# Performance work log

Measured on AMD Instinct MI355X. Metric: run time of the kernel, lower is better.

The kernel has to match this reference:

```python
import jax, jax.numpy as jnp
import numpy as np

UNITS = 128  # rnn_units hardcoded in the module


def setup_inputs() -> dict:
    key = jax.random.key(0)
    k1, k2, k3 = jax.random.split(key, 3)
    B, T, F = 256, 1024, 128  # feature dim must equal UNITS (shared cell across both layers)
    inputs = jax.random.normal(k1, (B, T, F), dtype=jnp.float32)
    # Keras LSTMCell params, gate order i|f|g|o; SHARED by both stacked layers
    # because StackedRNNCells([cell]*2) reuses the same cell object.
    W = jax.random.normal(k2, (F, 4 * UNITS), dtype=jnp.float32) * 0.05   # kernel
    U = jax.random.normal(k3, (UNITS, 4 * UNITS), dtype=jnp.float32) * 0.05  # recurrent_kernel
    b = jnp.zeros((4 * UNITS,), dtype=jnp.float32)  # bias
    return {"inputs": inputs, "W": W, "U": U, "b": b}


def _lstm_cell(x, h, c, W, U, b):
    # z: [B, 4*UNITS]; Keras gate order i, f, g(candidate), o
    z = x @ W + h @ U + b
    i, f, g, o = jnp.split(z, 4, axis=-1)
    i = jax.nn.sigmoid(i)
    f = jax.nn.sigmoid(f)
    g = jnp.tanh(g)
    o = jax.nn.sigmoid(o)
    c_new = f * c + i * g
    h_new = o * jnp.tanh(c_new)
    return h_new, c_new


def reference(inputs, W, U, b):
    B, T, F = inputs.shape
    z0 = jnp.zeros((B, UNITS), dtype=inputs.dtype)

    def step(carry, x_t):
        h1, c1, h2, c2 = carry
        h1, c1 = _lstm_cell(x_t, h1, c1, W, U, b)   # layer 1
        h2, c2 = _lstm_cell(h1, h2, c2, W, U, b)    # layer 2 (shared weights)
        return (h1, c1, h2, c2), None

    (h1, c1, h2, c2), _ = jax.lax.scan(step, (z0, z0, z0, z0), jnp.swapaxes(inputs, 0, 1))
    outputs = h2                                    # last-step output (return_sequences=False)
    init_state = jnp.zeros(inputs.shape, dtype=inputs.dtype)  # tf.zeros(inputs.shape)
    final_state = c1  # source unpacks `outputs, _, h2, _, _` -> 2nd flat state = layer-1 cell state
    return (outputs, init_state, final_state)
```

## Files before the change

### kernel.cpp

```cpp
#include <hip/hip_runtime.h>


typedef _Float16 f16;
typedef _Float16 f16x2 __attribute__((ext_vector_type(2)));
typedef _Float16 f16x8 __attribute__((ext_vector_type(8)));
typedef float    f32x4 __attribute__((ext_vector_type(4)));

#define T_STEPS 1024
#define UNITS   128
#define NB      32
#define BPW     8
#define NBLK    256
#define OUT_ZERO 32768
#define OUT_C1   33587200
#define BUFB     6144

__device__ __forceinline__ float frcp_(float x) {
#if __has_builtin(__builtin_amdgcn_rcpf)
    return __builtin_amdgcn_rcpf(x);
#else
    return 1.0f / x;
#endif
}
__device__ __forceinline__ float sigmoidf_(float x) {
    return frcp_(1.0f + __expf(-x));
}
__device__ __forceinline__ float tanhf_(float x) {
    float e = __expf(2.0f * x);
    return 1.0f - 2.0f * frcp_(e + 1.0f);
}
__device__ __forceinline__ unsigned pkh(float a, float b) {
    f16x2 t; t[0] = (f16)a; t[1] = (f16)b;
    return __builtin_bit_cast(unsigned, t);
}

__global__ __launch_bounds__(512, 2) void lstm2_kernel(
    const float* __restrict__ X,
    const float* __restrict__ W,
    const float* __restrict__ U,
    const float* __restrict__ Bv,
    float* __restrict__ out)
{
    const int blk = blockIdx.x;
    const int tid = threadIdx.x;

    if (blk >= NB) {
        const size_t nthr = (size_t)(NBLK - NB) * 512;
        float4* dst = (float4*)(out + OUT_ZERO);
        const float4 z4 = make_float4(0.f, 0.f, 0.f, 0.f);
        for (size_t i = (size_t)(blk - NB) * 512 + tid; i < 8388608u; i += nthr)
            dst[i] = z4;
        return;
    }

    const int wv = tid >> 6;
    const int l  = tid & 63;
    const int lr = l & 15;
    const int lc = l >> 4;
    const int u  = wv * 16 + lr;
    const int b0 = blk * BPW;
    const bool cell2 = (l >= 32);

    __shared__ __align__(16) char Abuf[2][BUFB];
    char* Ab = (char*)Abuf;

    f16x8 Wf[4][4], Uf[4][4];
    #pragma unroll
    for (int g = 0; g < 4; ++g) {
        #pragma unroll
        for (int kt = 0; kt < 4; ++kt) {
            f16x8 wt, ut;
            #pragma unroll
            for (int j = 0; j < 8; ++j) {
                const int krow = kt * 32 + lc * 8 + j;
                wt[j] = (f16)W[(size_t)krow * 512 + g * 128 + u];
                ut[j] = (f16)U[(size_t)krow * 512 + g * 128 + u];
            }
            Wf[g][kt] = wt;  Uf[g][kt] = ut;
        }
    }
    float bias[4];
    #pragma unroll
    for (int g = 0; g < 4; ++g) bias[g] = Bv[g * 128 + u];

    const int swz = (lr & 7) << 4;
    int raddr[2][4];
    #pragma unroll
    for (int a0 = 0; a0 < 2; ++a0)
        #pragma unroll
        for (int kt = 0; kt < 4; ++kt)
            raddr[a0][kt] = (((a0 * 8 + lr) * 256) + kt * 64 + lc * 16) ^ swz;
    int waddr[4];
    #pragma unroll
    for (int e = 0; e < 4; ++e)
        waddr[e] = ((8 + 4 * lc + e) * 256 + u * 2) ^ ((((4 * lc + e) & 7)) << 4);

    for (int i = tid; i < 3072; i += 512) ((float*)Ab)[i] = 0.0f;
    {
        const int flat = tid * 2, xr = flat >> 7, xc = flat & 127;
        const float2 xv = *(const float2*)(X + (size_t)(b0 + xr) * (T_STEPS * UNITS) + xc);
        const int byte = ((xr * 256 + xc * 2) ^ ((xr & 7) << 4));
        *(unsigned*)(Ab + byte) = pkh(xv.x, xv.y);
    }
    __syncthreads();

    float cst[4] = {0.f, 0.f, 0.f, 0.f};

    for (int k = 0; k <= T_STEPS; ++k) {
        const int rdo = (k & 1) * BUFB, wro = BUFB - rdo;

        float xa = 0.f, xb = 0.f; int xr = 0, xc = 0;
        if (k + 1 < T_STEPS) {
            const int flat = tid * 2; xr = flat >> 7; xc = flat & 127;
            const float2 xv = *(const float2*)(X + (size_t)(b0 + xr) * (T_STEPS * UNITS)
                                                 + (size_t)(k + 1) * UNITS + xc);
            xa = xv.x; xb = xv.y;
        }

        f16x8 A1[4], A2[4];
        #pragma unroll
        for (int kt = 0; kt < 4; ++kt) {
            A1[kt] = *(const f16x8*)(Ab + rdo + raddr[0][kt]);
            A2[kt] = *(const f16x8*)(Ab + rdo + raddr[1][kt]);
        }

        f32x4 acc[4];
        #pragma unroll
        for (int g = 0; g < 4; ++g) acc[g] = f32x4{0.f, 0.f, 0.f, 0.f};
        #pragma unroll
        for (int kt = 0; kt < 4; ++kt)
            #pragma unroll
            for (int g = 0; g < 4; ++g)
                acc[g] = __builtin_amdgcn_mfma_f32_16x16x32_f16(A1[kt], Wf[g][kt], acc[g], 0, 0, 0);
        #pragma unroll
        for (int kt = 0; kt < 4; ++kt)
            #pragma unroll
            for (int g = 0; g < 4; ++g)
                acc[g] = __builtin_amdgcn_mfma_f32_16x16x32_f16(A2[kt], Uf[g][kt], acc[g], 0, 0, 0);

        const bool active = cell2 ? (k > 0) : (k < T_STEPS);
        float hq[4];
        #pragma unroll
        for (int e = 0; e < 4; ++e) {
            const float zi = acc[0][e] + bias[0];
            const float zf = acc[1][e] + bias[1];
            const float zg = acc[2][e] + bias[2];
            const float zo = acc[3][e] + bias[3];
            const float ig = sigmoidf_(zi), fg = sigmoidf_(zf);
            const float gg = tanhf_(zg),    og = sigmoidf_(zo);
            const float cn = fg * cst[e] + ig * gg;
            if (active) cst[e] = cn;
            hq[e] = og * tanhf_(cn);
        }

        if (active && k < T_STEPS) {
            #pragma unroll
            for (int e = 0; e < 4; ++e)
                *(f16*)(Ab + wro + waddr[e]) = (f16)hq[e];
        }
        if (k + 1 < T_STEPS) {
            const int byte = ((xr * 256 + xc * 2) ^ ((xr & 7) << 4));
            *(unsigned*)(Ab + wro + byte) = pkh(xa, xb);
        }

        if (k == T_STEPS - 1 && !cell2) {
            #pragma unroll
            for (int e = 0; e < 4; ++e)
                out[OUT_C1 + (size_t)(b0 + 4 * lc + e) * UNITS + u] = cst[e];
        }
        if (k == T_STEPS && cell2) {
            #pragma unroll
            for (int e = 0; e < 4; ++e)
                out[(size_t)(b0 + 4 * lc + e - 8) * UNITS + u] = hq[e];
        }
        __syncthreads();
    }
}

extern "C" void kernel_launch(void* const* d_in, const int* in_sizes, int n_in,
                              void* d_out, int out_size, void* d_ws, size_t ws_size,
                              hipStream_t stream) {
    const float* X  = (const float*)d_in[0];
    const float* W  = (const float*)d_in[1];
    const float* U  = (const float*)d_in[2];
    const float* Bv = (const float*)d_in[3];
    float* out = (float*)d_out;
    hipLaunchKernelGGL(lstm2_kernel, dim3(NBLK), dim3(512), 0, stream,
                       X, W, U, Bv, out);
}
```

Measured before the change: 1.186 ms.

## Use 64 LSTM blocks with 4 batches each and a fused K=256 MFMA

```diff
diff --git a/kernel.cpp b/kernel.cpp
--- a/kernel.cpp
+++ b/kernel.cpp
@@ -8,12 +8,13 @@
 
 #define T_STEPS 1024
 #define UNITS   128
-#define NB      32
-#define BPW     8
+#define NLSTM   64
+#define BPW     4
 #define NBLK    256
 #define OUT_ZERO 32768
 #define OUT_C1   33587200
-#define BUFB     6144
+#define ROWB    512
+#define ABUF_B  (16*ROWB)
 
 __device__ __forceinline__ float frcp_(float x) {
 #if __has_builtin(__builtin_amdgcn_rcpf)
@@ -33,6 +34,13 @@
     f16x2 t; t[0] = (f16)a; t[1] = (f16)b;
     return __builtin_bit_cast(unsigned, t);
 }
+__device__ __forceinline__ unsigned short hbits(float a) {
+    f16 t = (f16)a;
+    return __builtin_bit_cast(unsigned short, t);
+}
+__device__ __forceinline__ int swb(int row, int byteoff) {
+    return row * ROWB + ((((byteoff >> 4) ^ (row & 7)) << 4) | (byteoff & 15));
+}
 
 __global__ __launch_bounds__(512, 2) void lstm2_kernel(
     const float* __restrict__ X,
@@ -44,135 +52,124 @@
     const int blk = blockIdx.x;
     const int tid = threadIdx.x;
 
-    if (blk >= NB) {
-        const size_t nthr = (size_t)(NBLK - NB) * 512;
+    if (blk >= NLSTM) {
+        const size_t nthr = (size_t)(NBLK - NLSTM) * 512;
         float4* dst = (float4*)(out + OUT_ZERO);
         const float4 z4 = make_float4(0.f, 0.f, 0.f, 0.f);
-        for (size_t i = (size_t)(blk - NB) * 512 + tid; i < 8388608u; i += nthr)
+        for (size_t i = (size_t)(blk - NLSTM) * 512 + tid; i < 8388608u; i += nthr)
             dst[i] = z4;
         return;
     }
 
-    const int wv = tid >> 6;
+    const int w  = tid >> 6;
     const int l  = tid & 63;
     const int lr = l & 15;
     const int lc = l >> 4;
-    const int u  = wv * 16 + lr;
+    const int u  = w * 16 + lr;
     const int b0 = blk * BPW;
-    const bool cell2 = (l >= 32);
 
-    __shared__ __align__(16) char Abuf[2][BUFB];
-    char* Ab = (char*)Abuf;
+    __shared__ __align__(16) char   Ab[2][ABUF_B];
+    __shared__ __align__(16) float4 zlds[8][129];
 
-    f16x8 Wf[4][4], Uf[4][4];
+    f16x8 Bf[4][8];
     #pragma unroll
     for (int g = 0; g < 4; ++g) {
         #pragma unroll
-        for (int kt = 0; kt < 4; ++kt) {
-            f16x8 wt, ut;
+        for (int kt = 0; kt < 8; ++kt) {
+            f16x8 t;
             #pragma unroll
             for (int j = 0; j < 8; ++j) {
-                const int krow = kt * 32 + lc * 8 + j;
-                wt[j] = (f16)W[(size_t)krow * 512 + g * 128 + u];
-                ut[j] = (f16)U[(size_t)krow * 512 + g * 128 + u];
+                const int kg = kt * 32 + lc * 8 + j;
+                const float v = (kg < 128) ? W[(size_t)kg * 512 + g * 128 + u]
+                                           : U[(size_t)(kg - 128) * 512 + g * 128 + u];
+                t[j] = (f16)v;
             }
-            Wf[g][kt] = wt;  Uf[g][kt] = ut;
+            Bf[g][kt] = t;
         }
     }
     float bias[4];
     #pragma unroll
     for (int g = 0; g < 4; ++g) bias[g] = Bv[g * 128 + u];
 
-    const int swz = (lr & 7) << 4;
-    int raddr[2][4];
-    #pragma unroll
-    for (int a0 = 0; a0 < 2; ++a0)
-        #pragma unroll
-        for (int kt = 0; kt < 4; ++kt)
-            raddr[a0][kt] = (((a0 * 8 + lr) * 256) + kt * 64 + lc * 16) ^ swz;
-    int waddr[4];
-    #pragma unroll
-    for (int e = 0; e < 4; ++e)
-        waddr[e] = ((8 + 4 * lc + e) * 256 + u * 2) ^ ((((4 * lc + e) & 7)) << 4);
-
-    for (int i = tid; i < 3072; i += 512) ((float*)Ab)[i] = 0.0f;
-    {
+    for (int i = tid; i < 2 * ABUF_B / 16; i += 512) ((float4*)Ab)[i] = make_float4(0.f,0.f,0.f,0.f);
+    __syncthreads();
+    if (tid < 256) {
         const int flat = tid * 2, xr = flat >> 7, xc = flat & 127;
         const float2 xv = *(const float2*)(X + (size_t)(b0 + xr) * (T_STEPS * UNITS) + xc);
-        const int byte = ((xr * 256 + xc * 2) ^ ((xr & 7) << 4));
-        *(unsigned*)(Ab + byte) = pkh(xv.x, xv.y);
+        *(unsigned*)(&Ab[0][0] + swb(xr, xc * 2)) = pkh(xv.x, xv.y);
     }
     __syncthreads();
 
-    float cst[4] = {0.f, 0.f, 0.f, 0.f};
+    int ard[8];
+    #pragma unroll
+    for (int kt = 0; kt < 8; ++kt) ard[kt] = swb(lr, kt * 64 + lc * 16);
+
+    float c1 = 0.f, c2 = 0.f;
 
     for (int k = 0; k <= T_STEPS; ++k) {
-        const int rdo = (k & 1) * BUFB, wro = BUFB - rdo;
+        const int rdo = (k & 1) * ABUF_B, wro = ABUF_B - rdo;
+        char* Abr = &Ab[0][0] + rdo;
+        char* Abw = &Ab[0][0] + wro;
 
         float xa = 0.f, xb = 0.f; int xr = 0, xc = 0;
-        if (k + 1 < T_STEPS) {
+        if (tid < 256 && k + 1 < T_STEPS) {
             const int flat = tid * 2; xr = flat >> 7; xc = flat & 127;
             const float2 xv = *(const float2*)(X + (size_t)(b0 + xr) * (T_STEPS * UNITS)
                                                  + (size_t)(k + 1) * UNITS + xc);
             xa = xv.x; xb = xv.y;
         }
 
-        f16x8 A1[4], A2[4];
+        f16x8 Af[8];
         #pragma unroll
-        for (int kt = 0; kt < 4; ++kt) {
-            A1[kt] = *(const f16x8*)(Ab + rdo + raddr[0][kt]);
-            A2[kt] = *(const f16x8*)(Ab + rdo + raddr[1][kt]);
-        }
+        for (int kt = 0; kt < 8; ++kt) Af[kt] = *(const f16x8*)(Abr + ard[kt]);
 
         f32x4 acc[4];
         #pragma unroll
         for (int g = 0; g < 4; ++g) acc[g] = f32x4{0.f, 0.f, 0.f, 0.f};
         #pragma unroll
-        for (int kt = 0; kt < 4; ++kt)
+        for (int kt = 0; kt < 8; ++kt)
             #pragma unroll
             for (int g = 0; g < 4; ++g)
-                acc[g] = __builtin_amdgcn_mfma_f32_16x16x32_f16(A1[kt], Wf[g][kt], acc[g], 0, 0, 0);
-        #pragma unroll
-        for (int kt = 0; kt < 4; ++kt)
-            #pragma unroll
-            for (int g = 0; g < 4; ++g)
-                acc[g] = __builtin_amdgcn_mfma_f32_16x16x32_f16(A2[kt], Uf[g][kt], acc[g], 0, 0, 0);
+                acc[g] = __builtin_amdgcn_mfma_f32_16x16x32_f16(Af[kt], Bf[g][kt], acc[g], 0, 0, 0);
 
-        const bool active = cell2 ? (k > 0) : (k < T_STEPS);
-        float hq[4];
-        #pragma unroll
-        for (int e = 0; e < 4; ++e) {
-            const float zi = acc[0][e] + bias[0];
-            const float zf = acc[1][e] + bias[1];
-            const float zg = acc[2][e] + bias[2];
-            const float zo = acc[3][e] + bias[3];
-            const float ig = sigmoidf_(zi), fg = sigmoidf_(zf);
-            const float gg = tanhf_(zg),    og = sigmoidf_(zo);
-            const float cn = fg * cst[e] + ig * gg;
-            if (active) cst[e] = cn;
-            hq[e] = og * tanhf_(cn);
-        }
-
-        if (active && k < T_STEPS) {
+        if (lc < 2) {
             #pragma unroll
             for (int e = 0; e < 4; ++e)
-                *(f16*)(Ab + wro + waddr[e]) = (f16)hq[e];
+                zlds[4 * lc + e][u] = make_float4(acc[0][e], acc[1][e], acc[2][e], acc[3][e]);
         }
-        if (k + 1 < T_STEPS) {
-            const int byte = ((xr * 256 + xc * 2) ^ ((xr & 7) << 4));
-            *(unsigned*)(Ab + wro + byte) = pkh(xa, xb);
+        __syncthreads();
+
+        const float4 z1 = *(const float4*)&zlds[lc][u];
+        const float4 z2 = *(const float4*)&zlds[4 + lc][u];
+
+        if (k < T_STEPS) {
+            const float i1 = sigmoidf_(z1.x + bias[0]);
+            const float f1 = sigmoidf_(z1.y + bias[1]);
+            const float g1 = tanhf_(z1.z + bias[2]);
+            const float o1 = sigmoidf_(z1.w + bias[3]);
+            c1 = f1 * c1 + i1 * g1;
+            const float h1v = o1 * tanhf_(c1);
+            const unsigned short hb = hbits(h1v);
+            *(unsigned short*)(Abw + swb(lc,     256 + u * 2)) = hb;
+            *(unsigned short*)(Abw + swb(4 + lc, u * 2))       = hb;
+            if (k == T_STEPS - 1)
+                out[OUT_C1 + (size_t)(b0 + lc) * UNITS + u] = c1;
         }
+        if (k > 0) {
+            const float i2 = sigmoidf_(z2.x + bias[0]);
+            const float f2 = sigmoidf_(z2.y + bias[1]);
+            const float g2 = tanhf_(z2.z + bias[2]);
+            const float o2 = sigmoidf_(z2.w + bias[3]);
+            c2 = f2 * c2 + i2 * g2;
+            const float h2v = o2 * tanhf_(c2);
+            if (k < T_STEPS)
+                *(unsigned short*)(Abw + swb(4 + lc, 256 + u * 2)) = hbits(h2v);
+            else
+                out[(size_t)(b0 + lc) * UNITS + u] = h2v;
+        }
+        if (tid < 256 && k + 1 < T_STEPS)
+            *(unsigned*)(Abw + swb(xr, xc * 2)) = pkh(xa, xb);
 
-        if (k == T_STEPS - 1 && !cell2) {
-            #pragma unroll
-            for (int e = 0; e < 4; ++e)
-                out[OUT_C1 + (size_t)(b0 + 4 * lc + e) * UNITS + u] = cst[e];
-        }
-        if (k == T_STEPS && cell2) {
-            #pragma unroll
-            for (int e = 0; e < 4; ++e)
-                out[(size_t)(b0 + 4 * lc + e - 8) * UNITS + u] = hq[e];
-        }
         __syncthreads();
     }
 }
```

After: 1.394 ms. 17.5% more time.
